# Performance work log

Hardware: AMD Instinct MI355X
Metric: run time of the kernel (lower is better)

## Reference

```python
import jax, jax.numpy as jnp
import numpy as np

H = 1024
N_IDX = 400000
NBINS = 256


def setup_inputs() -> dict:
    key = jax.random.key(0)
    ks = jax.random.split(key, 10)
    return {
        "input_data": jax.random.uniform(ks[0], (1, 3, H, H), jnp.float32),
        "target_data": jax.random.uniform(ks[1], (1, 3, H, H), jnp.float32) * 2.0 - 1.0,
        "ref": jax.random.uniform(ks[2], (1, 3, H, H), jnp.float32) * 2.0 - 1.0,
        "mask_src": (jax.random.uniform(ks[3], (1, 1, H, H)) > 0.3).astype(jnp.float32) * 255.0,
        "mask_tar": (jax.random.uniform(ks[4], (1, 1, H, H)) > 0.3).astype(jnp.float32) * 255.0,
        "target_data_eye": jax.random.uniform(ks[5], (1, 3, H, H), jnp.float32),
        "idx0": jax.random.randint(ks[6], (N_IDX,), 0, H),
        "idx1": jax.random.randint(ks[7], (N_IDX,), 0, H),
        "idx2": jax.random.randint(ks[8], (N_IDX,), 0, H),
        "idx3": jax.random.randint(ks[9], (N_IDX,), 0, H),
    }


def _cdf(vals):
    # vals: [3, N] float in [0, 256). torch.histc(bins=256, min=0, max=256) -> bin = floor(v)
    bins = jnp.clip(vals.astype(jnp.int32), 0, NBINS - 1)  # [3, N]
    hist = jnp.zeros((3, NBINS), jnp.float32).at[jnp.arange(3)[:, None], bins].add(1.0)
    cdf = jnp.cumsum(hist, axis=1)
    return cdf / cdf[:, -1:]  # normalized cumulative histogram, [3, 256]


def _trans_table(cdf_dst, cdf_ref):
    # cal_trans(ref=cdf_dst, adj=cdf_ref): table[i] = first j in [1,255]
    # with cdf_ref[j-1] <= cdf_dst[i] <= cdf_ref[j]; else table[i] = i; table[255] = 255
    r = cdf_dst[:, None]                  # [256, 1]
    lo = cdf_ref[None, :-1]               # [1, 255] -> adj[j-1], j = 1..255
    hi = cdf_ref[None, 1:]                # [1, 255] -> adj[j]
    cond = (r >= lo) & (r <= hi)          # [256, 255]
    has = cond.any(axis=1)
    j = jnp.argmax(cond, axis=1) + 1      # first matching j
    table = jnp.where(has, j, jnp.arange(NBINS))
    return table.at[NBINS - 1].set(NBINS - 1)


def _hist_match(dst_img, ref_img, i0, i1, i2, i3):
    # dst_img, ref_img: [3, H, W]; gather masked pixels per channel
    dst_align = dst_img[:, i0, i1]        # [3, N]
    ref_align = ref_img[:, i2, i3]        # [3, N]
    cdf_dst = _cdf(dst_align)
    cdf_ref = _cdf(ref_align)
    tables = jax.vmap(_trans_table)(cdf_dst, cdf_ref)  # [3, 256] int
    bins = jnp.clip(dst_align.astype(jnp.int32), 0, NBINS - 1)  # int() truncation, v >= 0
    matched = jnp.take_along_axis(tables, bins, axis=1).astype(dst_img.dtype)  # [3, N]
    return dst_img.at[:, i0, i1].set(matched)


def reference(input_data, target_data, ref, mask_src, mask_tar, target_data_eye,
              idx0, idx1, idx2, idx3):
    # part = 'lip' (generic part) -> histogram_matching branch; use_vgg = False
    de_norm = lambda x: jnp.clip((x + 1.0) / 2.0, 0.0, 1.0)
    target = (de_norm(target_data) * 255.0)[0]          # [3, H, W]
    inp = (jnp.clip(input_data, 0.0, 1.0) * 255.0)[0]   # [3, H, W]
    r = (de_norm(ref) * 255.0)[0]                       # [3, H, W]
    msrc = jnp.broadcast_to(mask_src / 255.0, (1, 3, H, H))[0]
    mtar = jnp.broadcast_to(mask_tar / 255.0, (1, 3, H, H))[0]

    input_masked = inp * msrc
    target_masked = target * mtar
    ref_masked = r * msrc

    input_match = jax.lax.stop_gradient(
        _hist_match(ref_masked, target_masked, idx0, idx1, idx2, idx3))

    loss = jnp.mean(jnp.abs(input_masked / 255.0 - input_match / 255.0))
    return ((target_masked / 255.0)[None], (ref_masked / 255.0)[None],
            (input_masked / 255.0)[None], (input_match / 255.0)[None], loss)
```

## Files before the change

kernel.cpp:

```cpp
#include <hip/hip_runtime.h>

#define H 1024
#define HH (H * H)
#define CHW (3 * HH)
#define NB 256
#define HIST_BLOCKS 784

typedef float nfloat4 __attribute__((ext_vector_type(4)));

__device__ __forceinline__ float clamp01(float x) { return fminf(fmaxf(x, 0.0f), 1.0f); }

__device__ __forceinline__ unsigned int bin8(float v01) {
    int b = (int)(v01 * 255.0f);
    return (unsigned int)min(max(b, 0), NB - 1);
}

__device__ __forceinline__ void nt_store4(float4 v, float4* p) {
    nfloat4 nv; nv.x = v.x; nv.y = v.y; nv.z = v.z; nv.w = v.w;
    __builtin_nontemporal_store(nv, reinterpret_cast<nfloat4*>(p));
}

__global__ void k_elementwise(const float4* __restrict__ inp,
                              const float4* __restrict__ tar,
                              const float4* __restrict__ rfp,
                              const float4* __restrict__ msrc,
                              const float4* __restrict__ mtar,
                              float4* __restrict__ out0, float4* __restrict__ out1,
                              float4* __restrict__ out2, float4* __restrict__ out3,
                              uint4* __restrict__ pk_dst, uint4* __restrict__ pk_ref,
                              unsigned int* __restrict__ gz, float* __restrict__ loss)
{
    if (blockIdx.x == 0) {
        for (int i = threadIdx.x; i < 1537; i += blockDim.x) gz[i] = 0u;
        if (threadIdx.x == 0) *loss = 0.0f;
    }
    int p = blockIdx.x * blockDim.x + threadIdx.x;
    if (p >= HH / 4) return;
    float4 ms4 = msrc[p], mt4 = mtar[p];
    float msx = ms4.x / 255.0f, msy = ms4.y / 255.0f, msz = ms4.z / 255.0f, msw = ms4.w / 255.0f;
    float mtx = mt4.x / 255.0f, mty = mt4.y / 255.0f, mtz = mt4.z / 255.0f, mtw = mt4.w / 255.0f;
    unsigned int bd0 = 0, bd1 = 0, bd2 = 0, bd3 = 0;
    unsigned int br0 = 0, br1 = 0, br2 = 0, br3 = 0;
#pragma unroll
    for (int c = 0; c < 3; ++c) {
        int q = c * (HH / 4) + p;
        float4 t = tar[q], r = rfp[q], iv = inp[q];
        float4 o0, o1, o2;
        o0.x = clamp01((t.x + 1.0f) * 0.5f) * mtx;
        o0.y = clamp01((t.y + 1.0f) * 0.5f) * mty;
        o0.z = clamp01((t.z + 1.0f) * 0.5f) * mtz;
        o0.w = clamp01((t.w + 1.0f) * 0.5f) * mtw;
        o1.x = clamp01((r.x + 1.0f) * 0.5f) * msx;
        o1.y = clamp01((r.y + 1.0f) * 0.5f) * msy;
        o1.z = clamp01((r.z + 1.0f) * 0.5f) * msz;
        o1.w = clamp01((r.w + 1.0f) * 0.5f) * msw;
        o2.x = clamp01(iv.x) * msx;
        o2.y = clamp01(iv.y) * msy;
        o2.z = clamp01(iv.z) * msz;
        o2.w = clamp01(iv.w) * msw;
        nt_store4(o0, &out0[q]);
        nt_store4(o1, &out1[q]);
        out3[q] = o1;
        out2[q] = o2;
        int sh = 8 * c;
        bd0 |= bin8(o1.x) << sh;  bd1 |= bin8(o1.y) << sh;
        bd2 |= bin8(o1.z) << sh;  bd3 |= bin8(o1.w) << sh;
        br0 |= bin8(o0.x) << sh;  br1 |= bin8(o0.y) << sh;
        br2 |= bin8(o0.z) << sh;  br3 |= bin8(o0.w) << sh;
    }
    pk_dst[p] = make_uint4(bd0, bd1, bd2, bd3);
    pk_ref[p] = make_uint4(br0, br1, br2, br3);
}

__global__ void k_hist(const unsigned int* __restrict__ pk_dst,
                       const unsigned int* __restrict__ pk_ref,
                       const int* __restrict__ i0, const int* __restrict__ i1,
                       const int* __restrict__ i2, const int* __restrict__ i3,
                       unsigned int* __restrict__ ghist, unsigned int* __restrict__ counter,
                       float* __restrict__ table, int n)
{
    __shared__ unsigned int h[2 * 3 * NB];
    __shared__ float cdf[6][NB];
    __shared__ bool amLast;
    for (int i = threadIdx.x; i < 2 * 3 * NB; i += blockDim.x) h[i] = 0u;
    __syncthreads();

    for (int k = blockIdx.x * blockDim.x + threadIdx.x; k < n; k += gridDim.x * blockDim.x) {
        int pd = i0[k] * H + i1[k];
        int pr = i2[k] * H + i3[k];
        unsigned int a = pk_dst[pd];
        unsigned int b = pk_ref[pr];
        atomicAdd(&h[        (a       & 255u)], 1u);
        atomicAdd(&h[  NB + ((a >> 8) & 255u)], 1u);
        atomicAdd(&h[2*NB + ((a >>16) & 255u)], 1u);
        atomicAdd(&h[3*NB + ( b       & 255u)], 1u);
        atomicAdd(&h[4*NB + ((b >> 8) & 255u)], 1u);
        atomicAdd(&h[5*NB + ((b >>16) & 255u)], 1u);
    }
    __syncthreads();
    for (int i = threadIdx.x; i < 2 * 3 * NB; i += blockDim.x) {
        unsigned int v = h[i];
        if (v) atomicAdd(&ghist[i], v);
    }

    if (threadIdx.x == 0) {
        __threadfence();
        unsigned int old = atomicAdd(counter, 1u);
        amLast = (old == (unsigned int)(gridDim.x - 1));
    }
    __syncthreads();
    if (!amLast) return;

    int t = threadIdx.x;
    if (t < 384) {
        int wave = t >> 6, lane = t & 63;
        int base = wave * NB + lane * 4;
        unsigned int v0 = atomicAdd(&ghist[base + 0], 0u);
        unsigned int v1 = atomicAdd(&ghist[base + 1], 0u);
        unsigned int v2 = atomicAdd(&ghist[base + 2], 0u);
        unsigned int v3 = atomicAdd(&ghist[base + 3], 0u);
        unsigned int s0 = v0, s1 = s0 + v1, s2 = s1 + v2, s3 = s2 + v3;
        unsigned int scan = s3;
#pragma unroll
        for (int off = 1; off < 64; off <<= 1) {
            unsigned int u = (unsigned int)__shfl_up((int)scan, off, 64);
            if (lane >= off) scan += u;
        }
        unsigned int prefix = scan - s3;
        unsigned int total  = (unsigned int)__shfl((int)scan, 63, 64);
        float ft = (float)total;
        cdf[wave][lane * 4 + 0] = (float)(prefix + s0) / ft;
        cdf[wave][lane * 4 + 1] = (float)(prefix + s1) / ft;
        cdf[wave][lane * 4 + 2] = (float)(prefix + s2) / ft;
        cdf[wave][lane * 4 + 3] = (float)(prefix + s3) / ft;
    }
    __syncthreads();
    if (t < NB) {
#pragma unroll
        for (int c = 0; c < 3; ++c) {
            float r = cdf[c][t];
            const float* cr = cdf[3 + c];
            int lo = 1, hi = NB - 1;
#pragma unroll
            for (int it = 0; it < 8; ++it) {
                int mid = (lo + hi) >> 1;
                if (cr[mid] >= r) hi = mid; else lo = mid + 1;
            }
            int jstar = lo - 1;
            int tab = (jstar == 0 && cr[0] > r) ? t : (jstar + 1);
            if (t == NB - 1) tab = NB - 1;
            table[c * NB + t] = (float)tab / 255.0f;
        }
    }
}

__global__ void k_scatter(const unsigned int* __restrict__ pk_dst,
                          const int* __restrict__ i0, const int* __restrict__ i1,
                          const float* __restrict__ table, float* __restrict__ out3, int n)
{
    __shared__ float tl[3 * NB];
    for (int i = threadIdx.x; i < 3 * NB; i += blockDim.x) tl[i] = table[i];
    __syncthreads();
    int k = blockIdx.x * blockDim.x + threadIdx.x;
    if (k >= n) return;
    int pd = i0[k] * H + i1[k];
    unsigned int a = pk_dst[pd];
    out3[         pd] = tl[        (a       & 255u)];
    out3[HH     + pd] = tl[  NB + ((a >> 8) & 255u)];
    out3[2 * HH + pd] = tl[2*NB + ((a >>16) & 255u)];
}

__global__ void k_loss(const float4* __restrict__ a, const float4* __restrict__ b,
                       float* __restrict__ loss)
{
    float s = 0.0f;
    int n4 = CHW / 4;
    for (int i = blockIdx.x * blockDim.x + threadIdx.x; i < n4; i += gridDim.x * blockDim.x) {
        float4 x = a[i], y = b[i];
        s += fabsf(x.x - y.x) + fabsf(x.y - y.y) + fabsf(x.z - y.z) + fabsf(x.w - y.w);
    }
#pragma unroll
    for (int off = 32; off > 0; off >>= 1) s += __shfl_down(s, off);
    __shared__ float ws[4];
    int lane = threadIdx.x & 63, w = threadIdx.x >> 6;
    if (lane == 0) ws[w] = s;
    __syncthreads();
    if (threadIdx.x == 0) {
        float tsum = ws[0] + ws[1] + ws[2] + ws[3];
        atomicAdd(loss, tsum * (1.0f / (float)CHW));
    }
}

extern "C" void kernel_launch(void* const* d_in, const int* in_sizes, int n_in,
                              void* d_out, int out_size, void* d_ws, size_t ws_size,
                              hipStream_t stream)
{
    const float* inp  = (const float*)d_in[0];
    const float* tar  = (const float*)d_in[1];
    const float* rfp  = (const float*)d_in[2];
    const float* msrc = (const float*)d_in[3];
    const float* mtar = (const float*)d_in[4];
    const int* i0 = (const int*)d_in[6];
    const int* i1 = (const int*)d_in[7];
    const int* i2 = (const int*)d_in[8];
    const int* i3 = (const int*)d_in[9];
    int n = in_sizes[6];

    float* out0 = (float*)d_out;
    float* out1 = out0 + CHW;
    float* out2 = out1 + CHW;
    float* out3 = out2 + CHW;
    float* loss = out3 + CHW;

    unsigned int* ghist   = (unsigned int*)d_ws;
    unsigned int* counter = ghist + 1536;
    float*        table   = (float*)((char*)d_ws + 8192);
    unsigned int* pk_dst  = (unsigned int*)((char*)d_ws + 16384);
    unsigned int* pk_ref  = pk_dst + HH;

    k_elementwise<<<(HH / 4 + 255) / 256, 256, 0, stream>>>(
        (const float4*)inp, (const float4*)tar, (const float4*)rfp,
        (const float4*)msrc, (const float4*)mtar,
        (float4*)out0, (float4*)out1, (float4*)out2, (float4*)out3,
        (uint4*)pk_dst, (uint4*)pk_ref, ghist, loss);

    k_hist<<<HIST_BLOCKS, 512, 0, stream>>>(pk_dst, pk_ref, i0, i1, i2, i3,
                                            ghist, counter, table, n);

    k_scatter<<<(n + 255) / 256, 256, 0, stream>>>(pk_dst, i0, i1, table, out3, n);

    k_loss<<<768, 256, 0, stream>>>((const float4*)out2, (const float4*)out3, loss);
}
```

Baseline: 198.9 us.

## Fuse histogram and scatter kernels via a grid-wide flag barrier

Merges the histogram/table kernel and the scatter kernel into one persistent kernel. The last block builds the lookup table, publishes it with a global flag, and all other blocks spin on that flag before doing a grid-stride scatter. This removes one kernel launch and the gap between the two kernels. It relies on all 784 blocks being co-resident, otherwise the spin could deadlock. Nontemporal stores in the elementwise kernel are also replaced by plain stores.

After: 265.9 us. 33.6% more time.

```diff
diff --git a/kernel.cpp b/kernel.cpp
--- a/kernel.cpp
+++ b/kernel.cpp
@@ -6,18 +6,11 @@
 #define NB 256
 #define HIST_BLOCKS 784
 
-typedef float nfloat4 __attribute__((ext_vector_type(4)));
-
 __device__ __forceinline__ float clamp01(float x) { return fminf(fmaxf(x, 0.0f), 1.0f); }
 
 __device__ __forceinline__ unsigned int bin8(float v01) {
     int b = (int)(v01 * 255.0f);
     return (unsigned int)min(max(b, 0), NB - 1);
-}
-
-__device__ __forceinline__ void nt_store4(float4 v, float4* p) {
-    nfloat4 nv; nv.x = v.x; nv.y = v.y; nv.z = v.z; nv.w = v.w;
-    __builtin_nontemporal_store(nv, reinterpret_cast<nfloat4*>(p));
 }
 
 __global__ void k_elementwise(const float4* __restrict__ inp,
@@ -31,7 +24,7 @@
                               unsigned int* __restrict__ gz, float* __restrict__ loss)
 {
     if (blockIdx.x == 0) {
-        for (int i = threadIdx.x; i < 1537; i += blockDim.x) gz[i] = 0u;
+        for (int i = threadIdx.x; i < 1538; i += blockDim.x) gz[i] = 0u;
         if (threadIdx.x == 0) *loss = 0.0f;
     }
     int p = blockIdx.x * blockDim.x + threadIdx.x;
@@ -58,8 +51,8 @@
         o2.y = clamp01(iv.y) * msy;
         o2.z = clamp01(iv.z) * msz;
         o2.w = clamp01(iv.w) * msw;
-        nt_store4(o0, &out0[q]);
-        nt_store4(o1, &out1[q]);
+        out0[q] = o0;
+        out1[q] = o1;
         out3[q] = o1;
         out2[q] = o2;
         int sh = 8 * c;
@@ -72,15 +65,17 @@
     pk_ref[p] = make_uint4(br0, br1, br2, br3);
 }
 
-__global__ void k_hist(const unsigned int* __restrict__ pk_dst,
-                       const unsigned int* __restrict__ pk_ref,
-                       const int* __restrict__ i0, const int* __restrict__ i1,
-                       const int* __restrict__ i2, const int* __restrict__ i3,
-                       unsigned int* __restrict__ ghist, unsigned int* __restrict__ counter,
-                       float* __restrict__ table, int n)
+__global__ void k_fused(const unsigned int* __restrict__ pk_dst,
+                        const unsigned int* __restrict__ pk_ref,
+                        const int* __restrict__ i0, const int* __restrict__ i1,
+                        const int* __restrict__ i2, const int* __restrict__ i3,
+                        unsigned int* __restrict__ ghist, unsigned int* __restrict__ counter,
+                        unsigned int* __restrict__ flag, float* __restrict__ table,
+                        float* __restrict__ out3, int n)
 {
     __shared__ unsigned int h[2 * 3 * NB];
     __shared__ float cdf[6][NB];
+    __shared__ float tl[3 * NB];
     __shared__ bool amLast;
     for (int i = threadIdx.x; i < 2 * 3 * NB; i += blockDim.x) h[i] = 0u;
     __syncthreads();
@@ -109,65 +104,71 @@
         amLast = (old == (unsigned int)(gridDim.x - 1));
     }
     __syncthreads();
-    if (!amLast) return;
-
-    int t = threadIdx.x;
-    if (t < 384) {
-        int wave = t >> 6, lane = t & 63;
-        int base = wave * NB + lane * 4;
-        unsigned int v0 = atomicAdd(&ghist[base + 0], 0u);
-        unsigned int v1 = atomicAdd(&ghist[base + 1], 0u);
-        unsigned int v2 = atomicAdd(&ghist[base + 2], 0u);
-        unsigned int v3 = atomicAdd(&ghist[base + 3], 0u);
-        unsigned int s0 = v0, s1 = s0 + v1, s2 = s1 + v2, s3 = s2 + v3;
-        unsigned int scan = s3;
-#pragma unroll
-        for (int off = 1; off < 64; off <<= 1) {
-            unsigned int u = (unsigned int)__shfl_up((int)scan, off, 64);
-            if (lane >= off) scan += u;
+
+    if (amLast) {
+        int t = threadIdx.x;
+        if (t < 384) {
+            int wave = t >> 6, lane = t & 63;
+            int base = wave * NB + lane * 4;
+            unsigned int v0 = atomicAdd(&ghist[base + 0], 0u);
+            unsigned int v1 = atomicAdd(&ghist[base + 1], 0u);
+            unsigned int v2 = atomicAdd(&ghist[base + 2], 0u);
+            unsigned int v3 = atomicAdd(&ghist[base + 3], 0u);
+            unsigned int s0 = v0, s1 = s0 + v1, s2 = s1 + v2, s3 = s2 + v3;
+            unsigned int scan = s3;
+#pragma unroll
+            for (int off = 1; off < 64; off <<= 1) {
+                unsigned int u = (unsigned int)__shfl_up((int)scan, off, 64);
+                if (lane >= off) scan += u;
+            }
+            unsigned int prefix = scan - s3;
+            unsigned int total  = (unsigned int)__shfl((int)scan, 63, 64);
+            float ft = (float)total;
+            cdf[wave][lane * 4 + 0] = (float)(prefix + s0) / ft;
+            cdf[wave][lane * 4 + 1] = (float)(prefix + s1) / ft;
+            cdf[wave][lane * 4 + 2] = (float)(prefix + s2) / ft;
+            cdf[wave][lane * 4 + 3] = (float)(prefix + s3) / ft;
         }
-        unsigned int prefix = scan - s3;
-        unsigned int total  = (unsigned int)__shfl((int)scan, 63, 64);
-        float ft = (float)total;
-        cdf[wave][lane * 4 + 0] = (float)(prefix + s0) / ft;
-        cdf[wave][lane * 4 + 1] = (float)(prefix + s1) / ft;
-        cdf[wave][lane * 4 + 2] = (float)(prefix + s2) / ft;
-        cdf[wave][lane * 4 + 3] = (float)(prefix + s3) / ft;
-    }
-    __syncthreads();
-    if (t < NB) {
-#pragma unroll
-        for (int c = 0; c < 3; ++c) {
-            float r = cdf[c][t];
-            const float* cr = cdf[3 + c];
-            int lo = 1, hi = NB - 1;
-#pragma unroll
-            for (int it = 0; it < 8; ++it) {
-                int mid = (lo + hi) >> 1;
-                if (cr[mid] >= r) hi = mid; else lo = mid + 1;
+        __syncthreads();
+        if (t < NB) {
+#pragma unroll
+            for (int c = 0; c < 3; ++c) {
+                float r = cdf[c][t];
+                const float* cr = cdf[3 + c];
+                int lo = 1, hi = NB - 1;
+#pragma unroll
+                for (int it = 0; it < 8; ++it) {
+                    int mid = (lo + hi) >> 1;
+                    if (cr[mid] >= r) hi = mid; else lo = mid + 1;
+                }
+                int jstar = lo - 1;
+                int tab = (jstar == 0 && cr[0] > r) ? t : (jstar + 1);
+                if (t == NB - 1) tab = NB - 1;
+                atomicExch(&table[c * NB + t], (float)tab / 255.0f);
             }
-            int jstar = lo - 1;
-            int tab = (jstar == 0 && cr[0] > r) ? t : (jstar + 1);
-            if (t == NB - 1) tab = NB - 1;
-            table[c * NB + t] = (float)tab / 255.0f;
         }
-    }
-}
-
-__global__ void k_scatter(const unsigned int* __restrict__ pk_dst,
-                          const int* __restrict__ i0, const int* __restrict__ i1,
-                          const float* __restrict__ table, float* __restrict__ out3, int n)
-{
-    __shared__ float tl[3 * NB];
-    for (int i = threadIdx.x; i < 3 * NB; i += blockDim.x) tl[i] = table[i];
-    __syncthreads();
-    int k = blockIdx.x * blockDim.x + threadIdx.x;
-    if (k >= n) return;
-    int pd = i0[k] * H + i1[k];
-    unsigned int a = pk_dst[pd];
-    out3[         pd] = tl[        (a       & 255u)];
-    out3[HH     + pd] = tl[  NB + ((a >> 8) & 255u)];
-    out3[2 * HH + pd] = tl[2*NB + ((a >>16) & 255u)];
+        __syncthreads();
+        if (t == 0) {
+            __threadfence();
+            atomicExch(flag, 1u);
+        }
+    }
+
+    if (threadIdx.x == 0) {
+        while (atomicAdd(flag, 0u) == 0u) { __builtin_amdgcn_s_sleep(8); }
+    }
+    __syncthreads();
+    for (int i = threadIdx.x; i < 3 * NB; i += blockDim.x)
+        tl[i] = atomicAdd(&table[i], 0.0f);
+    __syncthreads();
+
+    for (int k = blockIdx.x * blockDim.x + threadIdx.x; k < n; k += gridDim.x * blockDim.x) {
+        int pd = i0[k] * H + i1[k];
+        unsigned int a = pk_dst[pd];
+        out3[         pd] = tl[        (a       & 255u)];
+        out3[HH     + pd] = tl[  NB + ((a >> 8) & 255u)];
+        out3[2 * HH + pd] = tl[2*NB + ((a >>16) & 255u)];
+    }
 }
 
 __global__ void k_loss(const float4* __restrict__ a, const float4* __restrict__ b,
@@ -214,6 +215,7 @@
 
     unsigned int* ghist   = (unsigned int*)d_ws;
     unsigned int* counter = ghist + 1536;
+    unsigned int* flag    = ghist + 1537;
     float*        table   = (float*)((char*)d_ws + 8192);
     unsigned int* pk_dst  = (unsigned int*)((char*)d_ws + 16384);
     unsigned int* pk_ref  = pk_dst + HH;
@@ -224,10 +226,8 @@
         (float4*)out0, (float4*)out1, (float4*)out2, (float4*)out3,
         (uint4*)pk_dst, (uint4*)pk_ref, ghist, loss);
 
-    k_hist<<<HIST_BLOCKS, 512, 0, stream>>>(pk_dst, pk_ref, i0, i1, i2, i3,
-                                            ghist, counter, table, n);
-
-    k_scatter<<<(n + 255) / 256, 256, 0, stream>>>(pk_dst, i0, i1, table, out3, n);
+    k_fused<<<HIST_BLOCKS, 512, 0, stream>>>(pk_dst, pk_ref, i0, i1, i2, i3,
+                                             ghist, counter, flag, table, out3, n);
 
     k_loss<<<768, 256, 0, stream>>>((const float4*)out2, (const float4*)out3, loss);
 }
```
